# Performance work log

Hardware: AMD Instinct MI355X
Metric: run time of the kernel (lower is better)

Reference implementation:

```python
import jax, jax.numpy as jnp
import numpy as np

B, L, V, D, NCTX, DEPTH, VD = 4096, 77, 49408, 512, 4, 9, 768


def setup_inputs() -> dict:
    key = jax.random.key(0)
    ks = jax.random.split(key, 8)
    text = jax.random.randint(ks[0], (B, L), 0, V, dtype=jnp.int32)
    emb = jax.random.normal(ks[1], (V, D), dtype=jnp.float32) * 0.02
    ctx = jax.random.normal(ks[2], (NCTX, D), dtype=jnp.float32) * 0.02
    proj_w = jax.random.normal(ks[3], (VD, D), dtype=jnp.float32) * (1.0 / np.sqrt(D))
    proj_b = jnp.zeros((VD,), dtype=jnp.float32)
    cpt = jax.random.normal(ks[4], (DEPTH - 1, NCTX, D), dtype=jnp.float32) * 0.02
    cw = jax.random.normal(ks[5], (DEPTH - 1, VD, D), dtype=jnp.float32) * (1.0 / np.sqrt(D))
    cb = jnp.zeros((DEPTH - 1, VD), dtype=jnp.float32)
    return {"text": text, "emb": emb, "ctx": ctx, "proj_w": proj_w,
            "proj_b": proj_b, "cpt": cpt, "cw": cw, "cb": cb}


def _construct_prompts(text, emb, ctx):
    # Vectorized version of the per-token python loop in construct_prompts.
    b, l = text.shape
    n_ctx = ctx.shape[0]
    trunc = l - n_ctx - 1  # 77 - n_ctx - 1 tokens of the original sentence kept
    pt = jnp.zeros((b, l), dtype=text.dtype)
    pt = pt.at[:, 0].set(text[:, 0])                       # BOS
    pt = pt.at[:, n_ctx + 1:].set(text[:, 1:1 + trunc])    # shifted sentence
    # if the last slot is non-zero, replace with token at argmax position (EOT)
    ind = jnp.argmax(text, axis=-1)
    eot = jnp.take_along_axis(text, ind[:, None], axis=1)[:, 0]
    last = pt[:, -1]
    pt = pt.at[:, -1].set(jnp.where(last != 0, eot, last))
    # embedding gather, then scatter learned ctx into slots 1..1+n_ctx
    pe = emb[pt]  # [B, 77, D]
    pe = pe.at[:, 1:1 + n_ctx, :].set(jnp.broadcast_to(ctx, (b, n_ctx, ctx.shape[1])))
    return pe, pt.astype(jnp.float32)


def reference(text, emb, ctx, proj_w, proj_b, cpt, cw, cb):
    pe, pt = _construct_prompts(text, emb, ctx)
    proj_ctx = ctx @ proj_w.T + proj_b                      # [n_ctx, 768]
    vdp = jnp.einsum('knd,kod->kno', cpt, cw) + cb[:, None, :]  # [depth-1, n_ctx, 768]
    return (pe, pt, ctx, proj_ctx, cpt, vdp)
```

## Files before the change

kernel.cpp:

```cpp
#include <hip/hip_runtime.h>
#include <hip/hip_bf16.h>

#define BB   4096
#define LL   77
#define DD   512
#define NCTX 4
#define KK   8
#define VD   768

#define OFF_PE   0L
#define OFF_PT   161480704L
#define OFF_CTX  161796096L
#define OFF_PROJ 161798144L
#define OFF_CPT  161801216L
#define OFF_VDP  161817600L

__global__ __launch_bounds__(256) void k_build_pt(const int* __restrict__ text,
                                                  float* __restrict__ pt_f) {
    int gid  = blockIdx.x * 256 + threadIdx.x;
    int row  = gid >> 6;
    int lane = gid & 63;
    const int* t = text + row * LL;

    const int NEG = -2147483647 - 1;
    int v0 = (lane < LL)      ? t[lane]      : NEG;
    int v1 = (lane + 64 < LL) ? t[lane + 64] : NEG;
    int m  = v0 > v1 ? v0 : v1;
    #pragma unroll
    for (int off = 32; off; off >>= 1) {
        int o = __shfl_xor(m, off);
        m = o > m ? o : m;
    }

    float* dst = pt_f + (long)row * LL;
    #pragma unroll
    for (int pass = 0; pass < 2; ++pass) {
        int pos = lane + pass * 64;
        if (pos < LL) {
            int v;
            if (pos == 0)        v = t[0];
            else if (pos <= NCTX) v = 0;
            else if (pos == LL - 1) { int x = t[LL - 5]; v = (x != 0) ? m : 0; }
            else                 v = t[pos - NCTX];
            dst[pos] = (float)v;
        }
    }
}

__global__ __launch_bounds__(256) void k_gather_pe(const float4* __restrict__ emb,
                                                   const float4* __restrict__ ctx,
                                                   const float* __restrict__ pt_f,
                                                   float4* __restrict__ pe) {
    int t   = blockIdx.x * 256 + threadIdx.x;
    int row = t >> 7;
    int c   = t & 127;
    int pos = row % LL;

    const float4* src;
    if (pos >= 1 && pos <= NCTX) {
        src = ctx + (pos - 1) * (DD / 4);
    } else {
        int tok = (int)pt_f[row];
        src = emb + (long)tok * (DD / 4);
    }
    pe[t] = src[c];
}

__global__ __launch_bounds__(256) void k_small_dots(const float* __restrict__ ctx,
                                                    const float* __restrict__ proj_w,
                                                    const float* __restrict__ proj_b,
                                                    const float* __restrict__ cpt,
                                                    const float* __restrict__ cw,
                                                    const float* __restrict__ cb,
                                                    float* __restrict__ out) {
    int gid  = blockIdx.x * 256 + threadIdx.x;
    int wave = gid >> 6;
    int lane = gid & 63;

    const float* a;
    const float* b;
    float bias;
    float* dst;

    if (wave < NCTX * VD) {
        int n = wave / VD;
        int o = wave - n * VD;
        a    = ctx + n * DD;
        b    = proj_w + (long)o * DD;
        bias = proj_b[o];
        dst  = out + OFF_PROJ + wave;
    } else {
        int w = wave - NCTX * VD;
        int k = w / (NCTX * VD);
        int r = w - k * (NCTX * VD);
        int n = r / VD;
        int o = r - n * VD;
        a    = cpt + (long)(k * NCTX + n) * DD;
        b    = cw + (long)(k * VD + o) * DD;
        bias = cb[k * VD + o];
        dst  = out + OFF_VDP + w;
    }

    const float4* a4 = (const float4*)a + lane * 2;
    const float4* b4 = (const float4*)b + lane * 2;
    float4 x0 = a4[0], x1 = a4[1];
    float4 y0 = b4[0], y1 = b4[1];
    float s = x0.x * y0.x + x0.y * y0.y + x0.z * y0.z + x0.w * y0.w
            + x1.x * y1.x + x1.y * y1.y + x1.z * y1.z + x1.w * y1.w;
    #pragma unroll
    for (int off = 32; off; off >>= 1) s += __shfl_xor(s, off);
    if (lane == 0) *dst = s + bias;
}

extern "C" void kernel_launch(void* const* d_in, const int* in_sizes, int n_in,
                              void* d_out, int out_size, void* d_ws, size_t ws_size,
                              hipStream_t stream) {
    const int*   text   = (const int*)d_in[0];
    const float* emb    = (const float*)d_in[1];
    const float* ctx    = (const float*)d_in[2];
    const float* proj_w = (const float*)d_in[3];
    const float* proj_b = (const float*)d_in[4];
    const float* cpt    = (const float*)d_in[5];
    const float* cw     = (const float*)d_in[6];
    const float* cb     = (const float*)d_in[7];
    float* out = (float*)d_out;

    {
        int waves  = BB;
        int blocks = waves * 64 / 256;
        k_build_pt<<<blocks, 256, 0, stream>>>(text, out + OFF_PT);
    }

    {
        long threads = (long)BB * LL * 128;
        int  blocks  = (int)(threads / 256);
        k_gather_pe<<<blocks, 256, 0, stream>>>((const float4*)emb,
                                                (const float4*)ctx,
                                                out + OFF_PT,
                                                (float4*)(out + OFF_PE));
    }

    {
        int waves  = NCTX * VD + KK * NCTX * VD;
        int blocks = waves * 64 / 256;
        k_small_dots<<<blocks, 256, 0, stream>>>(ctx, proj_w, proj_b,
                                                 cpt, cw, cb, out);
    }

    hipMemcpyAsync(out + OFF_CTX, ctx, (size_t)NCTX * DD * sizeof(float),
                   hipMemcpyDeviceToDevice, stream);
    hipMemcpyAsync(out + OFF_CPT, cpt, (size_t)KK * NCTX * DD * sizeof(float),
                   hipMemcpyDeviceToDevice, stream);
}
```

Before: 808.9 us.

## Fuse small dots, token build and copies into one prep kernel; nontemporal gather

Merges the token-building kernel, the small projection dot kernel and the two device-to-device memcpys into a single prep kernel that picks its role from the block index. This removes three launches and two copy operations from the stream. The gather kernel now has each thread move two 16-byte chunks of a row and writes them with nontemporal stores, so the large pe output does not displace the embedding table from cache. The dot blocks now sit ahead of the token blocks on the critical path before the gather can start.

```diff
diff --git a/kernel.cpp b/kernel.cpp
--- a/kernel.cpp
+++ b/kernel.cpp
@@ -15,101 +15,126 @@
 #define OFF_CPT  161801216L
 #define OFF_VDP  161817600L
 
-__global__ __launch_bounds__(256) void k_build_pt(const int* __restrict__ text,
-                                                  float* __restrict__ pt_f) {
-    int gid  = blockIdx.x * 256 + threadIdx.x;
-    int row  = gid >> 6;
-    int lane = gid & 63;
-    const int* t = text + row * LL;
+typedef float f32x4 __attribute__((ext_vector_type(4)));
 
-    const int NEG = -2147483647 - 1;
-    int v0 = (lane < LL)      ? t[lane]      : NEG;
-    int v1 = (lane + 64 < LL) ? t[lane + 64] : NEG;
-    int m  = v0 > v1 ? v0 : v1;
-    #pragma unroll
-    for (int off = 32; off; off >>= 1) {
-        int o = __shfl_xor(m, off);
-        m = o > m ? o : m;
-    }
+#define DOT_BLOCKS 6912
+#define PT_BLOCKS  1024
+#define CPY_BLOCKS 18
 
-    float* dst = pt_f + (long)row * LL;
-    #pragma unroll
-    for (int pass = 0; pass < 2; ++pass) {
-        int pos = lane + pass * 64;
-        if (pos < LL) {
-            int v;
-            if (pos == 0)        v = t[0];
-            else if (pos <= NCTX) v = 0;
-            else if (pos == LL - 1) { int x = t[LL - 5]; v = (x != 0) ? m : 0; }
-            else                 v = t[pos - NCTX];
-            dst[pos] = (float)v;
+__global__ __launch_bounds__(256) void k_prep(const int* __restrict__ text,
+                                              const float* __restrict__ ctx,
+                                              const float* __restrict__ proj_w,
+                                              const float* __restrict__ proj_b,
+                                              const float* __restrict__ cpt,
+                                              const float* __restrict__ cw,
+                                              const float* __restrict__ cb,
+                                              float* __restrict__ out) {
+    int blk = blockIdx.x;
+    int tid = threadIdx.x;
+
+    if (blk < DOT_BLOCKS) {
+        int gid  = blk * 256 + tid;
+        int wave = gid >> 6;
+        int lane = gid & 63;
+
+        const float* a;
+        const float* b;
+        float bias;
+        float* dst;
+
+        if (wave < NCTX * VD) {
+            int n = wave / VD;
+            int o = wave - n * VD;
+            a    = ctx + n * DD;
+            b    = proj_w + (long)o * DD;
+            bias = proj_b[o];
+            dst  = out + OFF_PROJ + wave;
+        } else {
+            int w = wave - NCTX * VD;
+            int k = w / (NCTX * VD);
+            int r = w - k * (NCTX * VD);
+            int n = r / VD;
+            int o = r - n * VD;
+            a    = cpt + (long)(k * NCTX + n) * DD;
+            b    = cw + (long)(k * VD + o) * DD;
+            bias = cb[k * VD + o];
+            dst  = out + OFF_VDP + w;
+        }
+
+        const f32x4* a4 = (const f32x4*)a + lane * 2;
+        const f32x4* b4 = (const f32x4*)b + lane * 2;
+        f32x4 x0 = a4[0], x1 = a4[1];
+        f32x4 y0 = b4[0], y1 = b4[1];
+        float s = x0.x * y0.x + x0.y * y0.y + x0.z * y0.z + x0.w * y0.w
+                + x1.x * y1.x + x1.y * y1.y + x1.z * y1.z + x1.w * y1.w;
+        #pragma unroll
+        for (int off = 32; off; off >>= 1) s += __shfl_xor(s, off);
+        if (lane == 0) *dst = s + bias;
+
+    } else if (blk < DOT_BLOCKS + PT_BLOCKS) {
+        int gid  = (blk - DOT_BLOCKS) * 256 + tid;
+        int row  = gid >> 6;
+        int lane = gid & 63;
+        const int* t = text + row * LL;
+
+        const int NEG = -2147483647 - 1;
+        int v0 = (lane < LL)      ? t[lane]      : NEG;
+        int v1 = (lane + 64 < LL) ? t[lane + 64] : NEG;
+        int m  = v0 > v1 ? v0 : v1;
+        #pragma unroll
+        for (int off = 32; off; off >>= 1) {
+            int o = __shfl_xor(m, off);
+            m = o > m ? o : m;
+        }
+
+        float* dst = out + OFF_PT + (long)row * LL;
+        #pragma unroll
+        for (int pass = 0; pass < 2; ++pass) {
+            int pos = lane + pass * 64;
+            if (pos < LL) {
+                int v;
+                if (pos == 0)          v = t[0];
+                else if (pos <= NCTX)  v = 0;
+                else if (pos == LL - 1){ int x = t[LL - 5]; v = (x != 0) ? m : 0; }
+                else                   v = t[pos - NCTX];
+                dst[pos] = (float)v;
+            }
+        }
+
+    } else {
+        int i = (blk - DOT_BLOCKS - PT_BLOCKS) * 256 + tid;
+        const f32x4* c4  = (const f32x4*)ctx;
+        const f32x4* p4  = (const f32x4*)cpt;
+        f32x4* o4 = (f32x4*)out;
+        if (i < 512) {
+            o4[OFF_CTX / 4 + i] = c4[i];
+        } else {
+            o4[OFF_CPT / 4 + (i - 512)] = p4[i - 512];
         }
     }
 }
 
-__global__ __launch_bounds__(256) void k_gather_pe(const float4* __restrict__ emb,
-                                                   const float4* __restrict__ ctx,
-                                                   const float* __restrict__ pt_f,
-                                                   float4* __restrict__ pe) {
-    int t   = blockIdx.x * 256 + threadIdx.x;
-    int row = t >> 7;
-    int c   = t & 127;
-    int pos = row % LL;
+__global__ __launch_bounds__(256) void k_gather(const f32x4* __restrict__ emb,
+                                                const f32x4* __restrict__ ctx,
+                                                const float* __restrict__ pt_f,
+                                                f32x4* __restrict__ pe) {
+    int t    = blockIdx.x * 256 + threadIdx.x;
+    int row  = t >> 6;
+    int lane = t & 63;
+    int pos  = row % LL;
 
-    const float4* src;
+    const f32x4* src;
     if (pos >= 1 && pos <= NCTX) {
         src = ctx + (pos - 1) * (DD / 4);
     } else {
         int tok = (int)pt_f[row];
         src = emb + (long)tok * (DD / 4);
     }
-    pe[t] = src[c];
-}
-
-__global__ __launch_bounds__(256) void k_small_dots(const float* __restrict__ ctx,
-                                                    const float* __restrict__ proj_w,
-                                                    const float* __restrict__ proj_b,
-                                                    const float* __restrict__ cpt,
-                                                    const float* __restrict__ cw,
-                                                    const float* __restrict__ cb,
-                                                    float* __restrict__ out) {
-    int gid  = blockIdx.x * 256 + threadIdx.x;
-    int wave = gid >> 6;
-    int lane = gid & 63;
-
-    const float* a;
-    const float* b;
-    float bias;
-    float* dst;
-
-    if (wave < NCTX * VD) {
-        int n = wave / VD;
-        int o = wave - n * VD;
-        a    = ctx + n * DD;
-        b    = proj_w + (long)o * DD;
-        bias = proj_b[o];
-        dst  = out + OFF_PROJ + wave;
-    } else {
-        int w = wave - NCTX * VD;
-        int k = w / (NCTX * VD);
-        int r = w - k * (NCTX * VD);
-        int n = r / VD;
-        int o = r - n * VD;
-        a    = cpt + (long)(k * NCTX + n) * DD;
-        b    = cw + (long)(k * VD + o) * DD;
-        bias = cb[k * VD + o];
-        dst  = out + OFF_VDP + w;
-    }
-
-    const float4* a4 = (const float4*)a + lane * 2;
-    const float4* b4 = (const float4*)b + lane * 2;
-    float4 x0 = a4[0], x1 = a4[1];
-    float4 y0 = b4[0], y1 = b4[1];
-    float s = x0.x * y0.x + x0.y * y0.y + x0.z * y0.z + x0.w * y0.w
-            + x1.x * y1.x + x1.y * y1.y + x1.z * y1.z + x1.w * y1.w;
-    #pragma unroll
-    for (int off = 32; off; off >>= 1) s += __shfl_xor(s, off);
-    if (lane == 0) *dst = s + bias;
+    f32x4 a = src[lane];
+    f32x4 b = src[lane + 64];
+    f32x4* dst = pe + (long)row * (DD / 4);
+    __builtin_nontemporal_store(a, dst + lane);
+    __builtin_nontemporal_store(b, dst + lane + 64);
 }
 
 extern "C" void kernel_launch(void* const* d_in, const int* in_sizes, int n_in,
@@ -125,30 +150,15 @@
     const float* cb     = (const float*)d_in[7];
     float* out = (float*)d_out;
 
-    {
-        int waves  = BB;
-        int blocks = waves * 64 / 256;
-        k_build_pt<<<blocks, 256, 0, stream>>>(text, out + OFF_PT);
-    }
+    k_prep<<<DOT_BLOCKS + PT_BLOCKS + CPY_BLOCKS, 256, 0, stream>>>(
+        text, ctx, proj_w, proj_b, cpt, cw, cb, out);
 
     {
-        long threads = (long)BB * LL * 128;
+        long threads = (long)BB * LL * 64;
         int  blocks  = (int)(threads / 256);
-        k_gather_pe<<<blocks, 256, 0, stream>>>((const float4*)emb,
-                                                (const float4*)ctx,
-                                                out + OFF_PT,
-                                                (float4*)(out + OFF_PE));
+        k_gather<<<blocks, 256, 0, stream>>>((const f32x4*)emb,
+                                             (const f32x4*)ctx,
+                                             out + OFF_PT,
+                                             (f32x4*)(out + OFF_PE));
     }
-
-    {
-        int waves  = NCTX * VD + KK * NCTX * VD;
-        int blocks = waves * 64 / 256;
-        k_small_dots<<<blocks, 256, 0, stream>>>(ctx, proj_w, proj_b,
-                                                 cpt, cw, cb, out);
-    }
-
-    hipMemcpyAsync(out + OFF_CTX, ctx, (size_t)NCTX * DD * sizeof(float),
-                   hipMemcpyDeviceToDevice, stream);
-    hipMemcpyAsync(out + OFF_CPT, cpt, (size_t)KK * NCTX * DD * sizeof(float),
-                   hipMemcpyDeviceToDevice, stream);
 }
```

Measured after the change: 758.8 us. 6.2% less time.
